# Kernel tuning notes

Hardware: AMD Instinct MI355X
Metric: run time of the kernel (lower is better)

## Reference

```python
import jax, jax.numpy as jnp
import numpy as np

B, C, H, W = 8, 64, 64, 64
MID = C // 8  # = 8, single-head key/query dim


def setup_inputs() -> dict:
    key = jax.random.key(0)
    ks = jax.random.split(key, 8)
    return {
        "x": jax.random.normal(ks[0], (B, C, H, W), dtype=jnp.float32),
        "wq": jax.random.normal(ks[1], (MID, C), dtype=jnp.float32) * 0.1,
        "bq": jax.random.normal(ks[2], (MID,), dtype=jnp.float32) * 0.1,
        "wk": jax.random.normal(ks[3], (MID, C), dtype=jnp.float32) * 0.1,
        "bk": jax.random.normal(ks[4], (MID,), dtype=jnp.float32) * 0.1,
        "wv": jax.random.normal(ks[5], (C, C), dtype=jnp.float32) * 0.1,
        "bv": jax.random.normal(ks[6], (C,), dtype=jnp.float32) * 0.1,
        "gamma": jax.random.uniform(ks[7], (1,), dtype=jnp.float32),
    }


def reference(x, wq, bq, wk, bk, wv, bv, gamma):
    b, c, h, w = x.shape
    n = h * w
    xf = x.reshape(b, c, n)  # [B, C, N]
    # 1x1 convs == per-pixel linear projections
    q = jnp.einsum("mc,bcn->bmn", wq, xf) + bq[:, None]  # [B, MID, N]
    k = jnp.einsum("mc,bcn->bmn", wk, xf) + bk[:, None]  # [B, MID, N]
    v = jnp.einsum("dc,bcn->bdn", wv, xf) + bv[:, None]  # [B, C, N]
    # attn[b, i, j] = softmax_j( q[:, i] . k[:, j] )  -- no scaling (SAGAN)
    attn = jax.nn.softmax(jnp.einsum("bmi,bmj->bij", q, k), axis=-1)  # [B, N, N]
    # out[b, c, i] = sum_j v[b, c, j] * attn[b, i, j]
    out = jnp.einsum("bcj,bij->bci", v, attn).reshape(b, c, h, w)
    return x + gamma[0] * out
```

## Files before the change

### kernel.cpp

```cpp
#include <hip/hip_runtime.h>
#include <math.h>

#define NB 8
#define NC 64
#define NN 4096
#define PS 72
#define LOG2E 1.4426950408889634f

typedef __attribute__((ext_vector_type(8))) short short8;
typedef __attribute__((ext_vector_type(4))) float float4v;

#if __has_builtin(__builtin_amdgcn_exp2f)
#define EXP2F(v) __builtin_amdgcn_exp2f(v)
#else
#define EXP2F(v) exp2f(v)
#endif

__device__ inline unsigned short f2bf(float f) {
    unsigned int u = __builtin_bit_cast(unsigned int, f);
    unsigned int r = (u + 0x7FFFu + ((u >> 16) & 1u)) >> 16;
    return (unsigned short)r;
}
__device__ inline unsigned int bfpack(float lo, float hi) {
    unsigned int a = __builtin_bit_cast(unsigned int, lo) + 0x8000u;
    unsigned int b = __builtin_bit_cast(unsigned int, hi) + 0x8000u;
    return __builtin_amdgcn_perm(b, a, 0x07060302u);
}

__global__ __launch_bounds__(256) void prepack_kernel(
    const float* __restrict__ wq, const float* __restrict__ bq,
    const float* __restrict__ wk, const float* __restrict__ bk,
    const float* __restrict__ wv, const float* __restrict__ bv,
    unsigned short* __restrict__ wpack, float* __restrict__ bpack)
{
    const int tid = threadIdx.x;
    for (int item = tid; item < 640; item += 256) {
        const int f = item >> 6, lane = item & 63;
        const int mt = f >> 1, kc = f & 1;
        const int c0 = lane & 15, quad = lane >> 4;
        const float* row;
        float scale = 1.f;
        if (mt < 4) row = wv + (mt * 16 + c0) * 64;
        else if (c0 < 8) { row = wq + c0 * 64; scale = LOG2E; }
        else row = wk + (c0 - 8) * 64;
        unsigned short* dst = wpack + ((size_t)f * 64 + lane) * 8;
        for (int e = 0; e < 8; ++e) dst[e] = f2bf(row[kc * 32 + quad * 8 + e] * scale);
    }
    if (tid < 80) {
        float v;
        if (tid < 64) v = bv[tid];
        else if (tid < 72) v = bq[tid - 64] * LOG2E;
        else v = bk[tid - 72];
        bpack[tid] = v;
    }
}

__global__ __launch_bounds__(64) void proj_mfma_kernel(
    const float* __restrict__ x,
    const unsigned short* __restrict__ wpack, const float* __restrict__ bpack,
    unsigned short* __restrict__ qo8, unsigned short* __restrict__ ko8,
    unsigned short* __restrict__ vo)
{
    const int b = blockIdx.y;
    const int lane = threadIdx.x;
    const int c0 = lane & 15, quad = lane >> 4;
    const int n0 = blockIdx.x * 16;

    __shared__ unsigned short qkb[16][24];

    short8 wf[10];
#pragma unroll
    for (int f = 0; f < 10; ++f)
        wf[f] = *(const short8*)(wpack + ((size_t)f * 64 + lane) * 8);

    const float* xb = x + (size_t)b * NC * NN + n0 + c0;
    short8 xf[2];
#pragma unroll
    for (int kc = 0; kc < 2; ++kc)
#pragma unroll
        for (int e = 0; e < 8; ++e)
            xf[kc][e] = (short)f2bf(xb[(size_t)(kc * 32 + quad * 8 + e) * NN]);

#pragma unroll
    for (int mt = 0; mt < 4; ++mt) {
        float4v acc = {0.f, 0.f, 0.f, 0.f};
        acc = __builtin_amdgcn_mfma_f32_16x16x32_bf16(wf[mt * 2], xf[0], acc, 0, 0, 0);
        acc = __builtin_amdgcn_mfma_f32_16x16x32_bf16(wf[mt * 2 + 1], xf[1], acc, 0, 0, 0);
#pragma unroll
        for (int reg = 0; reg < 4; ++reg) {
            int ch = mt * 16 + quad * 4 + reg;
            vo[((size_t)b * NC + ch) * NN + n0 + c0] = f2bf(acc[reg] + bpack[ch]);
        }
    }
    {
        float4v acc = {0.f, 0.f, 0.f, 0.f};
        acc = __builtin_amdgcn_mfma_f32_16x16x32_bf16(wf[8], xf[0], acc, 0, 0, 0);
        acc = __builtin_amdgcn_mfma_f32_16x16x32_bf16(wf[9], xf[1], acc, 0, 0, 0);
        float a[4];
#pragma unroll
        for (int reg = 0; reg < 4; ++reg)
            a[reg] = acc[reg] + bpack[64 + quad * 4 + reg];
        *(uint2*)&qkb[c0][quad * 4] = make_uint2(bfpack(a[0], a[1]), bfpack(a[2], a[3]));
        if (quad == 0) {
            uint4 qrow = *(const uint4*)&qkb[c0][0];
            uint4 krow = *(const uint4*)&qkb[c0][8];
            *(uint4*)&qo8[((size_t)b * NN + n0 + c0) * 8] = qrow;
            *(uint4*)&ko8[((size_t)b * NN + n0 + c0) * 8] = krow;
        }
    }
}

__global__ __launch_bounds__(256, 4) void attn_fused_kernel(
    const unsigned short* __restrict__ qo8, const unsigned short* __restrict__ ko8,
    const unsigned short* __restrict__ vo,
    const float* __restrict__ x, const float* __restrict__ gamma,
    float* __restrict__ out)
{
    const int b = blockIdx.x;
    const int i0b = blockIdx.y * 32;
    const int wave = threadIdx.x >> 6, lane = threadIdx.x & 63;
    const int c0 = lane & 15, quad = lane >> 4;

    __shared__ unsigned int obuf[4][64][17];
    __shared__ float lbuf[4][2][16];

    unsigned short* psw = (unsigned short*)&obuf[wave][0][0];
    unsigned short* pswr = psw + c0 * PS + quad * 4;
    const unsigned short* psrd = psw + c0 * PS + quad * 8;

    const int jbase = wave * (NN / 4);

    short8 qf[2] = {};
    if (quad == 0) {
        qf[0] = *(const short8*)(qo8 + ((size_t)b * NN + i0b + c0) * 8);
        qf[1] = *(const short8*)(qo8 + ((size_t)b * NN + i0b + 16 + c0) * 8);
    } else if (quad == 1) {
        qf[0][0] = (short)0xC1E7;
        qf[1][0] = (short)0xC1E7;
    }
    short8 kcst = {};
    if (quad == 1) kcst[0] = (short)0x3F80;

    float4v acc[2][4];
#pragma unroll
    for (int qh = 0; qh < 2; ++qh)
#pragma unroll
        for (int ct = 0; ct < 4; ++ct) acc[qh][ct] = (float4v){0.f, 0.f, 0.f, 0.f};
    float lsum[2] = {0.f, 0.f};

    const unsigned short* vbase = vo + ((size_t)b * NC + c0) * NN + jbase + quad * 8;
    const unsigned short* kbase = ko8 + ((size_t)(b * NN + jbase + c0)) * 8;

    for (int t = 0; t < NN / 4 / 64; ++t) {
        const int jt = t * 64;
        short8 kf[4] = {kcst, kcst, kcst, kcst};
        if (quad == 0) {
#pragma unroll
            for (int st = 0; st < 4; ++st)
                kf[st] = *(const short8*)(kbase + (size_t)(jt + st * 16) * 8);
        }
        short8 vf[4][2];
#pragma unroll
        for (int ct = 0; ct < 4; ++ct)
#pragma unroll
            for (int kc = 0; kc < 2; ++kc)
                vf[ct][kc] = *(const short8*)(vbase + (size_t)ct * 16 * NN + jt + kc * 32);

#pragma unroll
        for (int qh = 0; qh < 2; ++qh) {
            float4v s[4];
#pragma unroll
            for (int st = 0; st < 4; ++st) {
                float4v z = {0.f, 0.f, 0.f, 0.f};
                s[st] = __builtin_amdgcn_mfma_f32_16x16x32_bf16(kf[st], qf[qh], z, 0, 0, 0);
            }
#pragma unroll
            for (int st = 0; st < 4; ++st) {
                float p0 = EXP2F(s[st][0]);
                float p1 = EXP2F(s[st][1]);
                float p2 = EXP2F(s[st][2]);
                float p3 = EXP2F(s[st][3]);
                lsum[qh] += (p0 + p1) + (p2 + p3);
                *(uint2*)(pswr + st * 16) = make_uint2(bfpack(p0, p1), bfpack(p2, p3));
            }
            {
                short8 pf0 = *(const short8*)(psrd);
#pragma unroll
                for (int ct = 0; ct < 4; ++ct)
                    acc[qh][ct] = __builtin_amdgcn_mfma_f32_16x16x32_bf16(
                        pf0, vf[ct][0], acc[qh][ct], 0, 0, 0);
                short8 pf1 = *(const short8*)(psrd + 32);
#pragma unroll
                for (int ct = 0; ct < 4; ++ct)
                    acc[qh][ct] = __builtin_amdgcn_mfma_f32_16x16x32_bf16(
                        pf1, vf[ct][1], acc[qh][ct], 0, 0, 0);
            }
        }
    }

#pragma unroll
    for (int qh = 0; qh < 2; ++qh) {
        lsum[qh] += __shfl_xor(lsum[qh], 16);
        lsum[qh] += __shfl_xor(lsum[qh], 32);
    }
    if (quad == 0) {
        lbuf[wave][0][c0] = lsum[0];
        lbuf[wave][1][c0] = lsum[1];
    }

#pragma unroll
    for (int qh = 0; qh < 2; ++qh)
#pragma unroll
        for (int ct = 0; ct < 4; ++ct) {
            const int ch = ct * 16 + c0;
            *(uint2*)&obuf[wave][ch][qh * 8 + quad * 2] =
                make_uint2(bfpack(acc[qh][ct][0], acc[qh][ct][1]),
                           bfpack(acc[qh][ct][2], acc[qh][ct][3]));
        }
    __syncthreads();

    const int q = threadIdx.x & 31;
    const int cg = threadIdx.x >> 5;
    const float L = lbuf[0][q >> 4][q & 15] + lbuf[1][q >> 4][q & 15] +
                    lbuf[2][q >> 4][q & 15] + lbuf[3][q >> 4][q & 15];
    const float scale = gamma[0] / L;
    const int d = ((q >> 4) << 3) | ((q & 12) >> 1) | ((q & 2) >> 1);
    const int sh = (q & 1) << 4;
    const size_t base = (size_t)b * NC * NN + i0b + q;
#pragma unroll
    for (int cc = 0; cc < 8; ++cc) {
        const int ch = cg * 8 + cc;
        float O = 0.f;
#pragma unroll
        for (int w = 0; w < 4; ++w)
            O += __builtin_bit_cast(float, (obuf[w][ch][d] >> sh) << 16);
        const size_t idx = base + (size_t)ch * NN;
        out[idx] = x[idx] + scale * O;
    }
}

extern "C" void kernel_launch(void* const* d_in, const int* in_sizes, int n_in,
                              void* d_out, int out_size, void* d_ws, size_t ws_size,
                              hipStream_t stream) {
    const float* x     = (const float*)d_in[0];
    const float* wq    = (const float*)d_in[1];
    const float* bq    = (const float*)d_in[2];
    const float* wk    = (const float*)d_in[3];
    const float* bk    = (const float*)d_in[4];
    const float* wv    = (const float*)d_in[5];
    const float* bv    = (const float*)d_in[6];
    const float* gamma = (const float*)d_in[7];
    float* out = (float*)d_out;

    float* bpack = (float*)d_ws;
    unsigned short* wpack = (unsigned short*)(bpack + 128);
    unsigned short* qo8 = wpack + 10 * 64 * 8;
    unsigned short* ko8 = qo8 + (size_t)NB * NN * 8;
    unsigned short* vo  = ko8 + (size_t)NB * NN * 8;

    prepack_kernel<<<1, 256, 0, stream>>>(wq, bq, wk, bk, wv, bv, wpack, bpack);
    proj_mfma_kernel<<<dim3(NN / 16, NB), 64, 0, stream>>>(x, wpack, bpack, qo8, ko8, vo);
    attn_fused_kernel<<<dim3(NB, NN / 32), 256, 0, stream>>>(qo8, ko8, vo, x, gamma, out);
}
```

Baseline: 150.2 us.

## Halve query tile per block and compute softmax row sums with MFMA

Each attention block now handles 16 query rows instead of 32. The grid doubles, shared memory per block shrinks, and launch bounds ask for 8 blocks per CU. The per-lane scalar exp-sum plus shuffle reduction is replaced by an extra MFMA of the probability tile against a ones vector. This also makes the row sums match the bf16-rounded probabilities. The trade-off is that every K and V tile load is now reused across half as many queries, so global and L2 traffic for K and V doubles in exchange for higher occupancy and lower register pressure.

```diff
diff --git a/kernel.cpp b/kernel.cpp
--- a/kernel.cpp
+++ b/kernel.cpp
@@ -110,19 +110,19 @@
     }
 }
 
-__global__ __launch_bounds__(256, 4) void attn_fused_kernel(
+__global__ __launch_bounds__(256, 8) void attn_fused_kernel(
     const unsigned short* __restrict__ qo8, const unsigned short* __restrict__ ko8,
     const unsigned short* __restrict__ vo,
     const float* __restrict__ x, const float* __restrict__ gamma,
     float* __restrict__ out)
 {
     const int b = blockIdx.x;
-    const int i0b = blockIdx.y * 32;
+    const int i0b = blockIdx.y * 16;
     const int wave = threadIdx.x >> 6, lane = threadIdx.x & 63;
     const int c0 = lane & 15, quad = lane >> 4;
 
-    __shared__ unsigned int obuf[4][64][17];
-    __shared__ float lbuf[4][2][16];
+    __shared__ unsigned int obuf[4][64][9];
+    __shared__ float lbuf[4][16];
 
     unsigned short* psw = (unsigned short*)&obuf[wave][0][0];
     unsigned short* pswr = psw + c0 * PS + quad * 4;
@@ -130,23 +130,21 @@
 
     const int jbase = wave * (NN / 4);
 
-    short8 qf[2] = {};
-    if (quad == 0) {
-        qf[0] = *(const short8*)(qo8 + ((size_t)b * NN + i0b + c0) * 8);
-        qf[1] = *(const short8*)(qo8 + ((size_t)b * NN + i0b + 16 + c0) * 8);
-    } else if (quad == 1) {
-        qf[0][0] = (short)0xC1E7;
-        qf[1][0] = (short)0xC1E7;
-    }
+    short8 qf = {};
+    if (quad == 0)
+        qf = *(const short8*)(qo8 + ((size_t)b * NN + i0b + c0) * 8);
+    else if (quad == 1)
+        qf[0] = (short)0xC1E7;
     short8 kcst = {};
     if (quad == 1) kcst[0] = (short)0x3F80;
 
-    float4v acc[2][4];
-#pragma unroll
-    for (int qh = 0; qh < 2; ++qh)
-#pragma unroll
-        for (int ct = 0; ct < 4; ++ct) acc[qh][ct] = (float4v){0.f, 0.f, 0.f, 0.f};
-    float lsum[2] = {0.f, 0.f};
+    short8 ones;
+#pragma unroll
+    for (int e = 0; e < 8; ++e) ones[e] = (short)0x3F80;
+
+    float4v acc[4], lacc = {0.f, 0.f, 0.f, 0.f};
+#pragma unroll
+    for (int ct = 0; ct < 4; ++ct) acc[ct] = (float4v){0.f, 0.f, 0.f, 0.f};
 
     const unsigned short* vbase = vo + ((size_t)b * NC + c0) * NN + jbase + quad * 8;
     const unsigned short* kbase = ko8 + ((size_t)(b * NN + jbase + c0)) * 8;
@@ -166,70 +164,53 @@
             for (int kc = 0; kc < 2; ++kc)
                 vf[ct][kc] = *(const short8*)(vbase + (size_t)ct * 16 * NN + jt + kc * 32);
 
-#pragma unroll
-        for (int qh = 0; qh < 2; ++qh) {
-            float4v s[4];
-#pragma unroll
-            for (int st = 0; st < 4; ++st) {
-                float4v z = {0.f, 0.f, 0.f, 0.f};
-                s[st] = __builtin_amdgcn_mfma_f32_16x16x32_bf16(kf[st], qf[qh], z, 0, 0, 0);
-            }
-#pragma unroll
-            for (int st = 0; st < 4; ++st) {
-                float p0 = EXP2F(s[st][0]);
-                float p1 = EXP2F(s[st][1]);
-                float p2 = EXP2F(s[st][2]);
-                float p3 = EXP2F(s[st][3]);
-                lsum[qh] += (p0 + p1) + (p2 + p3);
-                *(uint2*)(pswr + st * 16) = make_uint2(bfpack(p0, p1), bfpack(p2, p3));
-            }
-            {
-                short8 pf0 = *(const short8*)(psrd);
-#pragma unroll
-                for (int ct = 0; ct < 4; ++ct)
-                    acc[qh][ct] = __builtin_amdgcn_mfma_f32_16x16x32_bf16(
-                        pf0, vf[ct][0], acc[qh][ct], 0, 0, 0);
-                short8 pf1 = *(const short8*)(psrd + 32);
-#pragma unroll
-                for (int ct = 0; ct < 4; ++ct)
-                    acc[qh][ct] = __builtin_amdgcn_mfma_f32_16x16x32_bf16(
-                        pf1, vf[ct][1], acc[qh][ct], 0, 0, 0);
-            }
-        }
-    }
-
-#pragma unroll
-    for (int qh = 0; qh < 2; ++qh) {
-        lsum[qh] += __shfl_xor(lsum[qh], 16);
-        lsum[qh] += __shfl_xor(lsum[qh], 32);
-    }
-    if (quad == 0) {
-        lbuf[wave][0][c0] = lsum[0];
-        lbuf[wave][1][c0] = lsum[1];
-    }
-
-#pragma unroll
-    for (int qh = 0; qh < 2; ++qh)
-#pragma unroll
-        for (int ct = 0; ct < 4; ++ct) {
-            const int ch = ct * 16 + c0;
-            *(uint2*)&obuf[wave][ch][qh * 8 + quad * 2] =
-                make_uint2(bfpack(acc[qh][ct][0], acc[qh][ct][1]),
-                           bfpack(acc[qh][ct][2], acc[qh][ct][3]));
-        }
+        float4v s[4];
+#pragma unroll
+        for (int st = 0; st < 4; ++st) {
+            float4v z = {0.f, 0.f, 0.f, 0.f};
+            s[st] = __builtin_amdgcn_mfma_f32_16x16x32_bf16(kf[st], qf, z, 0, 0, 0);
+        }
+#pragma unroll
+        for (int st = 0; st < 4; ++st) {
+            float p0 = EXP2F(s[st][0]);
+            float p1 = EXP2F(s[st][1]);
+            float p2 = EXP2F(s[st][2]);
+            float p3 = EXP2F(s[st][3]);
+            *(uint2*)(pswr + st * 16) = make_uint2(bfpack(p0, p1), bfpack(p2, p3));
+        }
+#pragma unroll
+        for (int kc = 0; kc < 2; ++kc) {
+            short8 pf = *(const short8*)(psrd + kc * 32);
+#pragma unroll
+            for (int ct = 0; ct < 4; ++ct)
+                acc[ct] = __builtin_amdgcn_mfma_f32_16x16x32_bf16(
+                    pf, vf[ct][kc], acc[ct], 0, 0, 0);
+            lacc = __builtin_amdgcn_mfma_f32_16x16x32_bf16(pf, ones, lacc, 0, 0, 0);
+        }
+    }
+
+    if (c0 == 0) {
+#pragma unroll
+        for (int reg = 0; reg < 4; ++reg) lbuf[wave][quad * 4 + reg] = lacc[reg];
+    }
+#pragma unroll
+    for (int ct = 0; ct < 4; ++ct) {
+        const int ch = ct * 16 + c0;
+        *(uint2*)&obuf[wave][ch][quad * 2] =
+            make_uint2(bfpack(acc[ct][0], acc[ct][1]), bfpack(acc[ct][2], acc[ct][3]));
+    }
     __syncthreads();
 
-    const int q = threadIdx.x & 31;
-    const int cg = threadIdx.x >> 5;
-    const float L = lbuf[0][q >> 4][q & 15] + lbuf[1][q >> 4][q & 15] +
-                    lbuf[2][q >> 4][q & 15] + lbuf[3][q >> 4][q & 15];
+    const int q = threadIdx.x & 15;
+    const int cg = threadIdx.x >> 4;
+    const float L = lbuf[0][q] + lbuf[1][q] + lbuf[2][q] + lbuf[3][q];
     const float scale = gamma[0] / L;
-    const int d = ((q >> 4) << 3) | ((q & 12) >> 1) | ((q & 2) >> 1);
+    const int d = q >> 1;
     const int sh = (q & 1) << 4;
     const size_t base = (size_t)b * NC * NN + i0b + q;
 #pragma unroll
-    for (int cc = 0; cc < 8; ++cc) {
-        const int ch = cg * 8 + cc;
+    for (int cc = 0; cc < 4; ++cc) {
+        const int ch = cg * 4 + cc;
         float O = 0.f;
 #pragma unroll
         for (int w = 0; w < 4; ++w)
@@ -260,5 +241,5 @@
 
     prepack_kernel<<<1, 256, 0, stream>>>(wq, bq, wk, bk, wv, bv, wpack, bpack);
     proj_mfma_kernel<<<dim3(NN / 16, NB), 64, 0, stream>>>(x, wpack, bpack, qo8, ko8, vo);
-    attn_fused_kernel<<<dim3(NB, NN / 32), 256, 0, stream>>>(qo8, ko8, vo, x, gamma, out);
-}
+    attn_fused_kernel<<<dim3(NB, NN / 16), 256, 0, stream>>>(qo8, ko8, vo, x, gamma, out);
+}
```

Result: slower. 211.2 us (+40.7%).

## Stage V tiles into LDS via async global_load_lds with XOR-swizzled layout

Applied to the files above, without the earlier changes.

Each wave now loads its V tile for every 64-key step straight from global memory into a per-wave LDS buffer using the global_load_lds builtin. It then reads the MFMA operands back from LDS through an XOR-swizzled layout, replacing the earlier direct per-lane global loads into registers. The P scratch buffer is also swizzled, and both query halves share each V fragment read in a fused MFMA loop. The aim is better coalescing and fewer conflicts and vector registers. In exchange it adds LDS traffic, a full waitcnt each iteration with no double buffering, and a larger shared-memory footprint that may reduce occupancy.

```diff
diff --git a/kernel.cpp b/kernel.cpp
--- a/kernel.cpp
+++ b/kernel.cpp
@@ -4,7 +4,6 @@
 #define NB 8
 #define NC 64
 #define NN 4096
-#define PS 72
 #define LOG2E 1.4426950408889634f
 
 typedef __attribute__((ext_vector_type(8))) short short8;
@@ -15,6 +14,9 @@
 #else
 #define EXP2F(v) exp2f(v)
 #endif
+
+typedef const __attribute__((address_space(1))) void* gas_t;
+typedef __attribute__((address_space(3))) void* las_t;
 
 __device__ inline unsigned short f2bf(float f) {
     unsigned int u = __builtin_bit_cast(unsigned int, f);
@@ -120,13 +122,10 @@
     const int i0b = blockIdx.y * 32;
     const int wave = threadIdx.x >> 6, lane = threadIdx.x & 63;
     const int c0 = lane & 15, quad = lane >> 4;
-
-    __shared__ unsigned int obuf[4][64][17];
-    __shared__ float lbuf[4][2][16];
-
-    unsigned short* psw = (unsigned short*)&obuf[wave][0][0];
-    unsigned short* pswr = psw + c0 * PS + quad * 4;
-    const unsigned short* psrd = psw + c0 * PS + quad * 8;
+    const int key = c0 & 7;
+
+    __shared__ __align__(16) short vstage[4][4096];
+    __shared__ __align__(16) short ps[4][2048];
 
     const int jbase = wave * (NN / 4);
 
@@ -148,23 +147,36 @@
         for (int ct = 0; ct < 4; ++ct) acc[qh][ct] = (float4v){0.f, 0.f, 0.f, 0.f};
     float lsum[2] = {0.f, 0.f};
 
-    const unsigned short* vbase = vo + ((size_t)b * NC + c0) * NN + jbase + quad * 8;
+    const char* vsb = (const char*)vo +
+        (((size_t)(b * NC + (lane >> 3))) * NN + jbase +
+         (size_t)(((lane & 7) ^ ((lane >> 3) & 7)) * 8)) * 2;
     const unsigned short* kbase = ko8 + ((size_t)(b * NN + jbase + c0)) * 8;
 
-    for (int t = 0; t < NN / 4 / 64; ++t) {
-        const int jt = t * 64;
+    short* vsw = &vstage[wave][0];
+    short* psb = &ps[wave][0];
+    const int hb = quad >> 1, ql = quad & 1;
+    int pwoff[4];
+#pragma unroll
+    for (int st = 0; st < 4; ++st)
+        pwoff[st] = c0 * 64 + (((2 * st + hb) ^ key) * 8) + ql * 4;
+    const int g0 = (quad ^ key) * 8, g1 = ((4 + quad) ^ key) * 8;
+    const int proff[2] = {c0 * 64 + g0, c0 * 64 + g1};
+    const short* vr[2] = {vsw + c0 * 64 + g0, vsw + c0 * 64 + g1};
+
+#pragma unroll
+    for (int t = 0; t < 16; ++t) {
+#pragma unroll
+        for (int i = 0; i < 8; ++i)
+            __builtin_amdgcn_global_load_lds(
+                (gas_t)(const void*)(vsb + (size_t)i * 8 * NN * 2 + (size_t)t * 128),
+                (las_t)(void*)(vsw + i * 512), 16, 0, 0);
         short8 kf[4] = {kcst, kcst, kcst, kcst};
         if (quad == 0) {
 #pragma unroll
             for (int st = 0; st < 4; ++st)
-                kf[st] = *(const short8*)(kbase + (size_t)(jt + st * 16) * 8);
-        }
-        short8 vf[4][2];
-#pragma unroll
-        for (int ct = 0; ct < 4; ++ct)
-#pragma unroll
-            for (int kc = 0; kc < 2; ++kc)
-                vf[ct][kc] = *(const short8*)(vbase + (size_t)ct * 16 * NN + jt + kc * 32);
+                kf[st] = *(const short8*)(kbase + (size_t)(t * 64 + st * 16) * 8);
+        }
+        __builtin_amdgcn_s_waitcnt(0x0F70);
 
 #pragma unroll
         for (int qh = 0; qh < 2; ++qh) {
@@ -174,6 +186,7 @@
                 float4v z = {0.f, 0.f, 0.f, 0.f};
                 s[st] = __builtin_amdgcn_mfma_f32_16x16x32_bf16(kf[st], qf[qh], z, 0, 0, 0);
             }
+            short* pq = psb + qh * 1024;
 #pragma unroll
             for (int st = 0; st < 4; ++st) {
                 float p0 = EXP2F(s[st][0]);
@@ -181,19 +194,18 @@
                 float p2 = EXP2F(s[st][2]);
                 float p3 = EXP2F(s[st][3]);
                 lsum[qh] += (p0 + p1) + (p2 + p3);
-                *(uint2*)(pswr + st * 16) = make_uint2(bfpack(p0, p1), bfpack(p2, p3));
+                *(uint2*)(pq + pwoff[st]) = make_uint2(bfpack(p0, p1), bfpack(p2, p3));
             }
-            {
-                short8 pf0 = *(const short8*)(psrd);
-#pragma unroll
-                for (int ct = 0; ct < 4; ++ct)
-                    acc[qh][ct] = __builtin_amdgcn_mfma_f32_16x16x32_bf16(
-                        pf0, vf[ct][0], acc[qh][ct], 0, 0, 0);
-                short8 pf1 = *(const short8*)(psrd + 32);
-#pragma unroll
-                for (int ct = 0; ct < 4; ++ct)
-                    acc[qh][ct] = __builtin_amdgcn_mfma_f32_16x16x32_bf16(
-                        pf1, vf[ct][1], acc[qh][ct], 0, 0, 0);
+        }
+#pragma unroll
+        for (int kc = 0; kc < 2; ++kc) {
+            short8 pf0 = *(const short8*)(psb + proff[kc]);
+            short8 pf1 = *(const short8*)(psb + 1024 + proff[kc]);
+#pragma unroll
+            for (int ct = 0; ct < 4; ++ct) {
+                short8 vf = *(const short8*)(vr[kc] + ct * 1024);
+                acc[0][ct] = __builtin_amdgcn_mfma_f32_16x16x32_bf16(pf0, vf, acc[0][ct], 0, 0, 0);
+                acc[1][ct] = __builtin_amdgcn_mfma_f32_16x16x32_bf16(pf1, vf, acc[1][ct], 0, 0, 0);
             }
         }
     }
@@ -204,16 +216,15 @@
         lsum[qh] += __shfl_xor(lsum[qh], 32);
     }
     if (quad == 0) {
-        lbuf[wave][0][c0] = lsum[0];
-        lbuf[wave][1][c0] = lsum[1];
-    }
-
+        ((float*)psb)[c0] = lsum[0];
+        ((float*)psb)[16 + c0] = lsum[1];
+    }
 #pragma unroll
     for (int qh = 0; qh < 2; ++qh)
 #pragma unroll
         for (int ct = 0; ct < 4; ++ct) {
             const int ch = ct * 16 + c0;
-            *(uint2*)&obuf[wave][ch][qh * 8 + quad * 2] =
+            *(uint2*)&vsw[ch * 32 + (qh * 8 + quad * 2) * 2] =
                 make_uint2(bfpack(acc[qh][ct][0], acc[qh][ct][1]),
                            bfpack(acc[qh][ct][2], acc[qh][ct][3]));
         }
@@ -221,10 +232,11 @@
 
     const int q = threadIdx.x & 31;
     const int cg = threadIdx.x >> 5;
-    const float L = lbuf[0][q >> 4][q & 15] + lbuf[1][q >> 4][q & 15] +
-                    lbuf[2][q >> 4][q & 15] + lbuf[3][q >> 4][q & 15];
+    float L = 0.f;
+#pragma unroll
+    for (int w = 0; w < 4; ++w) L += ((const float*)&ps[w][0])[q];
     const float scale = gamma[0] / L;
-    const int d = ((q >> 4) << 3) | ((q & 12) >> 1) | ((q & 2) >> 1);
+    const int d = ((q >> 4) << 3) | ((q & 15) >> 1);
     const int sh = (q & 1) << 4;
     const size_t base = (size_t)b * NC * NN + i0b + q;
 #pragma unroll
@@ -233,7 +245,8 @@
         float O = 0.f;
 #pragma unroll
         for (int w = 0; w < 4; ++w)
-            O += __builtin_bit_cast(float, (obuf[w][ch][d] >> sh) << 16);
+            O += __builtin_bit_cast(float,
+                 ((((const unsigned int*)&vstage[w][0])[ch * 16 + d] >> sh) << 16));
         const size_t idx = base + (size_t)ch * NN;
         out[idx] = x[idx] + scale * O;
     }
```

New measurement: 202.0 us. 1.35x slower.
